# Kernel optimization log

Hardware: AMD Instinct MI355X
Metric: run time of the kernel (lower is better)

Reference implementation:

```python
import jax, jax.numpy as jnp
import numpy as np

N_EMBD = 1024
BLOCK_SIZE = 128
HEAD_SIZE = 128
THETA = 10000.0


def setup_inputs() -> dict:
    key = jax.random.key(0)
    k1, k2, k3, k4 = jax.random.split(key, 4)
    B, T = 256, BLOCK_SIZE
    x = jax.random.normal(k1, (B, T, N_EMBD), dtype=jnp.float32)
    # nn.Linear(n_embd, head_size, bias=False) stored as [n_embd, head_size] so y = x @ W
    s = 1.0 / np.sqrt(N_EMBD)
    Wq = jax.random.normal(k2, (N_EMBD, HEAD_SIZE), dtype=jnp.float32) * s
    Wk = jax.random.normal(k3, (N_EMBD, HEAD_SIZE), dtype=jnp.float32) * s
    Wv = jax.random.normal(k4, (N_EMBD, HEAD_SIZE), dtype=jnp.float32) * s
    return {"x": x, "Wq": Wq, "Wk": Wk, "Wv": Wv}


def _rope_cos_sin(T: int, head_size: int):
    # freqs = exp(arange(0, hs, 2) * (-log(theta)/hs)); angles = outer(t, freqs)
    inv_freq = jnp.exp(jnp.arange(0, head_size, 2, dtype=jnp.float32) * (-np.log(THETA) / head_size))
    angles = jnp.arange(T, dtype=jnp.float32)[:, None] * inv_freq[None, :]  # [T, hs/2]
    return jnp.cos(angles), jnp.sin(angles)


def _apply_rope(t, cos, sin):
    # complex-view rotation on interleaved (even, odd) pairs of the last dim
    tr = t[..., 0::2]  # real parts  [B,T,hs/2]
    ti = t[..., 1::2]  # imag parts
    out_r = tr * cos - ti * sin
    out_i = tr * sin + ti * cos
    return jnp.stack([out_r, out_i], axis=-1).reshape(t.shape)


def reference(x, Wq, Wk, Wv):
    B, T, _ = x.shape
    hs = Wq.shape[1]
    q = x @ Wq  # [B,T,hs]
    k = x @ Wk
    v = x @ Wv
    cos, sin = _rope_cos_sin(T, hs)
    q = _apply_rope(q, cos, sin)
    k = _apply_rope(k, cos, sin)
    scores = jnp.einsum('btd,bsd->bts', q, k) / jnp.sqrt(jnp.asarray(hs, q.dtype))
    causal = jnp.tril(jnp.ones((T, T), dtype=bool))
    scores = jnp.where(causal[None, :, :], scores, -jnp.inf)
    att = jax.nn.softmax(scores, axis=-1)  # dropout is identity in eval
    return jnp.einsum('bts,bsd->btd', att, v)
```

## Files before the change

kernel.cpp:

```cpp
#include <hip/hip_runtime.h>
#include <math.h>

typedef __bf16 bf16x8 __attribute__((ext_vector_type(8)));
typedef float  f32x4  __attribute__((ext_vector_type(4)));
typedef unsigned short us4 __attribute__((ext_vector_type(4)));

constexpr int N_EMBD = 1024;
constexpr int T_SEQ  = 128;
constexpr int HS     = 128;
constexpr int BATCH  = 256;
constexpr int ROWS   = BATCH * T_SEQ;

__device__ __forceinline__ void async16(const void* g, void* l) {
    __builtin_amdgcn_global_load_lds(
        (const __attribute__((address_space(1))) unsigned int*)g,
        (__attribute__((address_space(3))) unsigned int*)l, 16, 0, 0);
}
__device__ __forceinline__ unsigned short bfbits(float f) {
    return __builtin_bit_cast(unsigned short, (__bf16)f);
}
__device__ __forceinline__ f32x4 zero4() {
    f32x4 z = {0.f, 0.f, 0.f, 0.f};
    return z;
}

__global__ __launch_bounds__(256) void wcast(
    const float* __restrict__ Wq, const float* __restrict__ Wk,
    const float* __restrict__ Wv, unsigned short* __restrict__ Wt)
{
    __shared__ unsigned short tile[64][130];
    const int bid = blockIdx.x;
    const int nt  = bid >> 4;
    const int k0  = (bid & 15) << 6;
    const float* src = (nt == 0) ? Wq : ((nt == 1) ? Wk : Wv);
    const int tid = threadIdx.x;
#pragma unroll
    for (int j = 0; j < 32; ++j) {
        int idx = tid + j * 256;
        int k = idx >> 7, n = idx & 127;
        tile[k][n] = bfbits(src[(size_t)(k0 + k) * HS + n]);
    }
    __syncthreads();
#pragma unroll
    for (int j = 0; j < 32; ++j) {
        int idx = tid + j * 256;
        int n = idx >> 6, kk = idx & 63;
        Wt[(size_t)(nt * 128 + n) * N_EMBD + k0 + kk] = tile[kk][n];
    }
}

__global__ __launch_bounds__(512, 2) void head_fused(
    const float* __restrict__ x,
    const unsigned short* __restrict__ Wt,
    float* __restrict__ out)
{
    __shared__ char lds[139264];
    constexpr int QS = 0;
    constexpr int KS = 34816;
    constexpr int VS = 69632;
    constexpr int STG_A = 104448;
    constexpr int STG_B = 114688;

    const int tid  = threadIdx.x;
    const int w    = tid >> 6;
    const int l    = tid & 63;
    const int cl   = l & 15;
    const int quad = l >> 4;
    const int b    = blockIdx.x;
    const int row0 = b << 7;
    const int wm   = (w & 1) << 6;
    const int wn   = (w >> 1) * 96;

    const int arow = tid >> 2;
    const int acol = (tid & 3) << 3;
    const float* aptr = x + (size_t)(row0 + arow) * N_EMBD + acol;
    const int bsrc = (l & 3) ^ quad;

    f32x4 acc[4][6];
#pragma unroll
    for (int a = 0; a < 4; ++a)
#pragma unroll
        for (int c = 0; c < 6; ++c) acc[a][c] = zero4();

    f32x4 a0 = *(const f32x4*)(aptr);
    f32x4 a1 = *(const f32x4*)(aptr + 4);

    for (int kc = 0; kc < N_EMBD; kc += 32) {
        __syncthreads();
        bf16x8 aw;
        aw[0] = (__bf16)a0[0]; aw[1] = (__bf16)a0[1];
        aw[2] = (__bf16)a0[2]; aw[3] = (__bf16)a0[3];
        aw[4] = (__bf16)a1[0]; aw[5] = (__bf16)a1[1];
        aw[6] = (__bf16)a1[2]; aw[7] = (__bf16)a1[3];
        *(bf16x8*)(lds + STG_A + arow * 80 + (tid & 3) * 16) = aw;
#pragma unroll
        for (int jj = 0; jj < 3; ++jj) {
            int j = w * 3 + jj;
            int n = j * 16 + (l >> 2);
            async16(Wt + (size_t)n * N_EMBD + kc + bsrc * 8,
                    lds + STG_B + j * 1024 + 0);
        }
        __syncthreads();
        if (kc + 32 < N_EMBD) {
            a0 = *(const f32x4*)(aptr + kc + 32);
            a1 = *(const f32x4*)(aptr + kc + 36);
        }
        bf16x8 af[4], bf[6];
#pragma unroll
        for (int rt = 0; rt < 4; ++rt) {
            int m = wm + rt * 16 + cl;
            af[rt] = *(const bf16x8*)(lds + STG_A + m * 80 + quad * 16);
        }
#pragma unroll
        for (int ct = 0; ct < 6; ++ct) {
            int n = wn + ct * 16 + cl;
            bf[ct] = *(const bf16x8*)(lds + STG_B + n * 64 + ((quad ^ ((n >> 2) & 3)) << 4));
        }
#pragma unroll
        for (int rt = 0; rt < 4; ++rt)
#pragma unroll
            for (int ct = 0; ct < 6; ++ct)
                acc[rt][ct] = __builtin_amdgcn_mfma_f32_16x16x32_bf16(
                    af[rt], bf[ct], acc[rt][ct], 0, 0, 0);
    }

    const float LNT = 0.07195578430905272f;
#pragma unroll
    for (int ct = 0; ct < 6; ++ct) {
        int c0  = wn + ct * 16;
        int ntc = c0 >> 7;
        int d   = (c0 & 127) + cl;
        if (ntc < 2) {
            int qk = (ntc == 0) ? QS : KS;
            float freq = __expf(-(float)(d & ~1) * LNT);
#pragma unroll
            for (int rt = 0; rt < 4; ++rt) {
#pragma unroll
                for (int i = 0; i < 4; ++i) {
                    int t = wm + rt * 16 + quad * 4 + i;
                    float v = acc[rt][ct][i];
                    float p = __shfl_xor(v, 1);
                    float sn, cs;
                    __sincosf((float)t * freq, &sn, &cs);
                    float r = ((d & 1) == 0) ? (v * cs - p * sn) : (p * sn + v * cs);
                    *(unsigned short*)(lds + qk + t * 272 + d * 2) = bfbits(r);
                }
            }
        } else {
#pragma unroll
            for (int rt = 0; rt < 4; ++rt) {
                int s0 = wm + rt * 16 + quad * 4;
                us4 u;
                u.x = bfbits(acc[rt][ct][0]);
                u.y = bfbits(acc[rt][ct][1]);
                u.z = bfbits(acc[rt][ct][2]);
                u.w = bfbits(acc[rt][ct][3]);
                *(us4*)(lds + VS + d * 272 + s0 * 2) = u;
            }
        }
    }
    __syncthreads();

    const int nct = w + 1;
    const int nks = (w + 2) >> 1;
    char* pl = lds + STG_A + w * 4352;

    bf16x8 qf[4];
#pragma unroll
    for (int ks = 0; ks < 4; ++ks)
        qf[ks] = *(const bf16x8*)(lds + QS + (w * 16 + cl) * 272 + (ks * 4 + quad) * 16);

    f32x4 s[8];
#pragma unroll
    for (int ct = 0; ct < 8; ++ct) s[ct] = zero4();

#pragma unroll
    for (int ct = 0; ct < 8; ++ct) if (ct < nct) {
        const char* kr = lds + KS + (ct * 16 + cl) * 272;
#pragma unroll
        for (int ks = 0; ks < 4; ++ks) {
            bf16x8 bb = *(const bf16x8*)(kr + (ks * 4 + quad) * 16);
            s[ct] = __builtin_amdgcn_mfma_f32_16x16x32_bf16(qf[ks], bb, s[ct], 0, 0, 0);
        }
    }

    const float scale = 0.08838834764831845f;
#pragma unroll
    for (int i = 0; i < 4; ++i) {
        int t = w * 16 + quad * 4 + i;
        float mx = -3.0e38f;
#pragma unroll
        for (int ct = 0; ct < 8; ++ct) if (ct < nct) {
            int col = ct * 16 + cl;
            float v = s[ct][i] * scale;
            v = (col <= t) ? v : -INFINITY;
            s[ct][i] = v;
            mx = fmaxf(mx, v);
        }
        mx = fmaxf(mx, __shfl_xor(mx, 1));
        mx = fmaxf(mx, __shfl_xor(mx, 2));
        mx = fmaxf(mx, __shfl_xor(mx, 4));
        mx = fmaxf(mx, __shfl_xor(mx, 8));
        float sum = 0.f;
#pragma unroll
        for (int ct = 0; ct < 8; ++ct) if (ct < nct) {
            float p = __expf(s[ct][i] - mx);
            s[ct][i] = p;
            sum += p;
        }
        sum += __shfl_xor(sum, 1);
        sum += __shfl_xor(sum, 2);
        sum += __shfl_xor(sum, 4);
        sum += __shfl_xor(sum, 8);
        float inv = 1.0f / sum;
        int rl = quad * 4 + i;
#pragma unroll
        for (int ct = 0; ct < 8; ++ct) if (ct < nct) {
            *(unsigned short*)(pl + rl * 272 + (ct * 16 + cl) * 2) =
                bfbits(s[ct][i] * inv);
        }
        if ((w & 1) == 0) {
            *(unsigned short*)(pl + rl * 272 + (nct * 16 + cl) * 2) = 0;
        }
    }

    bf16x8 ap[4];
#pragma unroll
    for (int ks = 0; ks < 4; ++ks) if (ks < nks)
        ap[ks] = *(const bf16x8*)(pl + cl * 272 + (ks * 4 + quad) * 16);

    f32x4 o[8];
#pragma unroll
    for (int ct = 0; ct < 8; ++ct) o[ct] = zero4();

#pragma unroll
    for (int ct = 0; ct < 8; ++ct) {
        const char* vr = lds + VS + (ct * 16 + cl) * 272;
#pragma unroll
        for (int ks = 0; ks < 4; ++ks) if (ks < nks) {
            bf16x8 bb = *(const bf16x8*)(vr + (ks * 4 + quad) * 16);
            o[ct] = __builtin_amdgcn_mfma_f32_16x16x32_bf16(ap[ks], bb, o[ct], 0, 0, 0);
        }
    }

#pragma unroll
    for (int ct = 0; ct < 8; ++ct)
#pragma unroll
        for (int i = 0; i < 4; ++i) {
            int t = w * 16 + quad * 4 + i;
            out[(size_t)b * 16384 + (size_t)t * HS + ct * 16 + cl] = o[ct][i];
        }
}

extern "C" void kernel_launch(void* const* d_in, const int* in_sizes, int n_in,
                              void* d_out, int out_size, void* d_ws, size_t ws_size,
                              hipStream_t stream) {
    const float* x  = (const float*)d_in[0];
    const float* Wq = (const float*)d_in[1];
    const float* Wk = (const float*)d_in[2];
    const float* Wv = (const float*)d_in[3];
    float* out = (float*)d_out;

    unsigned short* Wt = (unsigned short*)d_ws;

    wcast<<<48, 256, 0, stream>>>(Wq, Wk, Wv, Wt);
    head_fused<<<BATCH, 512, 0, stream>>>(x, Wt, out);
}
```

Measured before the change: 228.4 us.

## Double-buffer the QKV projection GEMM with a 64-wide K step and prefetch

The fused QKV projection loop now uses a 64-element K step with double-buffered LDS tiles for x and the weights. The next weight tile is fetched with async global-to-LDS loads, and the next x tile is loaded into registers while MFMAs run on the current buffers. This leaves one barrier per iteration instead of two and widens the XOR swizzle of the weight tile. The aim is to hide global-load latency, since there is roughly one block per CU. The cost is more LDS (the staging buffers now overlap the Q/K/V regions) and more live registers for the prefetched data.

```diff
diff --git a/kernel.cpp b/kernel.cpp
--- a/kernel.cpp
+++ b/kernel.cpp
@@ -55,11 +55,12 @@
     float* __restrict__ out)
 {
     __shared__ char lds[139264];
-    constexpr int QS = 0;
-    constexpr int KS = 34816;
-    constexpr int VS = 69632;
-    constexpr int STG_A = 104448;
-    constexpr int STG_B = 114688;
+    constexpr int AST = 0,     ASZ = 18432;
+    constexpr int BST = 36864, BSZ = 49152;
+    constexpr int QS  = 0;
+    constexpr int KS  = 34816;
+    constexpr int VS  = 69632;
+    constexpr int PST = 104448;
 
     const int tid  = threadIdx.x;
     const int w    = tid >> 6;
@@ -71,10 +72,11 @@
     const int wm   = (w & 1) << 6;
     const int wn   = (w >> 1) * 96;
 
-    const int arow = tid >> 2;
-    const int acol = (tid & 3) << 3;
-    const float* aptr = x + (size_t)(row0 + arow) * N_EMBD + acol;
-    const int bsrc = (l & 3) ^ quad;
+    const int ar = tid >> 3;
+    const int ac = (tid & 7) << 3;
+    const float* aptr = x + (size_t)row0 * N_EMBD;
+    const int brow = l >> 3;
+    const int bxo  = ((l & 7) ^ brow) << 3;
 
     f32x4 acc[4][6];
 #pragma unroll
@@ -82,46 +84,88 @@
 #pragma unroll
         for (int c = 0; c < 6; ++c) acc[a][c] = zero4();
 
-    f32x4 a0 = *(const f32x4*)(aptr);
-    f32x4 a1 = *(const f32x4*)(aptr + 4);
-
-    for (int kc = 0; kc < N_EMBD; kc += 32) {
+    {
+#pragma unroll
+        for (int jj = 0; jj < 6; ++jj) {
+            int n = w * 48 + jj * 8 + brow;
+            async16(Wt + (size_t)n * N_EMBD + bxo,
+                    lds + BST + (w * 6 + jj) * 1024);
+        }
+        f32x4 p0[2], p1[2];
+#pragma unroll
+        for (int rr = 0; rr < 2; ++rr) {
+            const float* p = aptr + (size_t)(ar + rr * 64) * N_EMBD + ac;
+            p0[rr] = *(const f32x4*)p;
+            p1[rr] = *(const f32x4*)(p + 4);
+        }
+#pragma unroll
+        for (int rr = 0; rr < 2; ++rr) {
+            bf16x8 aw;
+            aw[0] = (__bf16)p0[rr][0]; aw[1] = (__bf16)p0[rr][1];
+            aw[2] = (__bf16)p0[rr][2]; aw[3] = (__bf16)p0[rr][3];
+            aw[4] = (__bf16)p1[rr][0]; aw[5] = (__bf16)p1[rr][1];
+            aw[6] = (__bf16)p1[rr][2]; aw[7] = (__bf16)p1[rr][3];
+            *(bf16x8*)(lds + AST + (ar + rr * 64) * 144 + ac * 2) = aw;
+        }
         __syncthreads();
-        bf16x8 aw;
-        aw[0] = (__bf16)a0[0]; aw[1] = (__bf16)a0[1];
-        aw[2] = (__bf16)a0[2]; aw[3] = (__bf16)a0[3];
-        aw[4] = (__bf16)a1[0]; aw[5] = (__bf16)a1[1];
-        aw[6] = (__bf16)a1[2]; aw[7] = (__bf16)a1[3];
-        *(bf16x8*)(lds + STG_A + arow * 80 + (tid & 3) * 16) = aw;
-#pragma unroll
-        for (int jj = 0; jj < 3; ++jj) {
-            int j = w * 3 + jj;
-            int n = j * 16 + (l >> 2);
-            async16(Wt + (size_t)n * N_EMBD + kc + bsrc * 8,
-                    lds + STG_B + j * 1024 + 0);
+    }
+
+    int cur = 0;
+#pragma unroll 2
+    for (int t = 0; t < 16; ++t) {
+        const int kc = (t + 1) << 6;
+        f32x4 p0[2], p1[2];
+        if (t < 15) {
+#pragma unroll
+            for (int rr = 0; rr < 2; ++rr) {
+                const float* p = aptr + (size_t)(ar + rr * 64) * N_EMBD + kc + ac;
+                p0[rr] = *(const f32x4*)p;
+                p1[rr] = *(const f32x4*)(p + 4);
+            }
+#pragma unroll
+            for (int jj = 0; jj < 6; ++jj) {
+                int n = w * 48 + jj * 8 + brow;
+                async16(Wt + (size_t)n * N_EMBD + kc + bxo,
+                        lds + BST + (cur ^ 1) * BSZ + (w * 6 + jj) * 1024);
+            }
+        }
+        const char* Ab = lds + AST + cur * ASZ;
+        const char* Bb = lds + BST + cur * BSZ;
+#pragma unroll
+        for (int ks2 = 0; ks2 < 2; ++ks2) {
+            bf16x8 af[4], bf[6];
+#pragma unroll
+            for (int rt = 0; rt < 4; ++rt)
+                af[rt] = *(const bf16x8*)(Ab + (wm + rt * 16 + cl) * 144
+                                          + ks2 * 64 + quad * 16);
+#pragma unroll
+            for (int ct = 0; ct < 6; ++ct) {
+                int n = wn + ct * 16 + cl;
+                bf[ct] = *(const bf16x8*)(Bb + n * 128
+                                          + (((ks2 * 4 + quad) ^ (n & 7)) << 4));
+            }
+#pragma unroll
+            for (int rt = 0; rt < 4; ++rt)
+#pragma unroll
+                for (int ct = 0; ct < 6; ++ct)
+                    acc[rt][ct] = __builtin_amdgcn_mfma_f32_16x16x32_bf16(
+                        af[rt], bf[ct], acc[rt][ct], 0, 0, 0);
+        }
+        if (t < 15) {
+            __builtin_amdgcn_sched_barrier(0);
+            char* An = lds + AST + (cur ^ 1) * ASZ;
+#pragma unroll
+            for (int rr = 0; rr < 2; ++rr) {
+                bf16x8 aw;
+                aw[0] = (__bf16)p0[rr][0]; aw[1] = (__bf16)p0[rr][1];
+                aw[2] = (__bf16)p0[rr][2]; aw[3] = (__bf16)p0[rr][3];
+                aw[4] = (__bf16)p1[rr][0]; aw[5] = (__bf16)p1[rr][1];
+                aw[6] = (__bf16)p1[rr][2]; aw[7] = (__bf16)p1[rr][3];
+                *(bf16x8*)(An + (ar + rr * 64) * 144 + ac * 2) = aw;
+            }
         }
         __syncthreads();
-        if (kc + 32 < N_EMBD) {
-            a0 = *(const f32x4*)(aptr + kc + 32);
-            a1 = *(const f32x4*)(aptr + kc + 36);
-        }
-        bf16x8 af[4], bf[6];
-#pragma unroll
-        for (int rt = 0; rt < 4; ++rt) {
-            int m = wm + rt * 16 + cl;
-            af[rt] = *(const bf16x8*)(lds + STG_A + m * 80 + quad * 16);
-        }
-#pragma unroll
-        for (int ct = 0; ct < 6; ++ct) {
-            int n = wn + ct * 16 + cl;
-            bf[ct] = *(const bf16x8*)(lds + STG_B + n * 64 + ((quad ^ ((n >> 2) & 3)) << 4));
-        }
-#pragma unroll
-        for (int rt = 0; rt < 4; ++rt)
-#pragma unroll
-            for (int ct = 0; ct < 6; ++ct)
-                acc[rt][ct] = __builtin_amdgcn_mfma_f32_16x16x32_bf16(
-                    af[rt], bf[ct], acc[rt][ct], 0, 0, 0);
+        cur ^= 1;
     }
 
     const float LNT = 0.07195578430905272f;
@@ -163,7 +207,7 @@
 
     const int nct = w + 1;
     const int nks = (w + 2) >> 1;
-    char* pl = lds + STG_A + w * 4352;
+    char* pl = lds + PST + w * 4352;
 
     bf16x8 qf[4];
 #pragma unroll
```

Measured after the change: 224.1 us. About the same (-1.9%).

## Split fused head kernel into double-buffered QKV+RoPE GEMM and separate attention kernel

Applied to the files above, without the earlier changes.

Splits the single fused per-batch kernel into two kernels. The first computes the QKV projection with RoPE over 64-row halves, using double-buffered LDS staging that prefetches the next K chunk during the MFMAs, and writes Q, K and transposed V to workspace as bf16. The second computes attention over 512 blocks of 4 waves, each wave handling one 16-row query segment and reading Q/K/V straight from global memory. This doubles the grid size and cuts LDS use to raise occupancy and overlap loads, at the cost of an extra kernel launch and a round trip of Q/K/V through global memory.

```diff
diff --git a/kernel.cpp b/kernel.cpp
--- a/kernel.cpp
+++ b/kernel.cpp
@@ -9,7 +9,6 @@
 constexpr int T_SEQ  = 128;
 constexpr int HS     = 128;
 constexpr int BATCH  = 256;
-constexpr int ROWS   = BATCH * T_SEQ;
 
 __device__ __forceinline__ void async16(const void* g, void* l) {
     __builtin_amdgcn_global_load_lds(
@@ -49,32 +48,32 @@
     }
 }
 
-__global__ __launch_bounds__(512, 2) void head_fused(
+__global__ __launch_bounds__(256, 2) void qkv_rope(
     const float* __restrict__ x,
     const unsigned short* __restrict__ Wt,
-    float* __restrict__ out)
+    unsigned short* __restrict__ qr,
+    unsigned short* __restrict__ kr,
+    unsigned short* __restrict__ vT)
 {
-    __shared__ char lds[139264];
-    constexpr int QS = 0;
-    constexpr int KS = 34816;
-    constexpr int VS = 69632;
-    constexpr int STG_A = 104448;
-    constexpr int STG_B = 114688;
+    __shared__ char lds[59392];
+    constexpr int AST = 0,     ASZ = 5120;
+    constexpr int BST = 10240, BSZ = 24576;
 
     const int tid  = threadIdx.x;
     const int w    = tid >> 6;
     const int l    = tid & 63;
     const int cl   = l & 15;
     const int quad = l >> 4;
-    const int b    = blockIdx.x;
-    const int row0 = b << 7;
-    const int wm   = (w & 1) << 6;
-    const int wn   = (w >> 1) * 96;
-
-    const int arow = tid >> 2;
-    const int acol = (tid & 3) << 3;
-    const float* aptr = x + (size_t)(row0 + arow) * N_EMBD + acol;
-    const int bsrc = (l & 3) ^ quad;
+    const int bx   = blockIdx.x;
+    const int b    = bx >> 1;
+    const int half = bx & 1;
+    const int row0 = b * 128 + half * 64;
+
+    const int ar = tid >> 2;
+    const int ac = (tid & 3) << 3;
+    const float* aptr = x + (size_t)(row0 + ar) * N_EMBD + ac;
+    const int brow = l >> 2;
+    const int bxo  = ((l & 3) ^ (brow & 3)) << 3;
 
     f32x4 acc[4][6];
 #pragma unroll
@@ -82,39 +81,49 @@
 #pragma unroll
         for (int c = 0; c < 6; ++c) acc[a][c] = zero4();
 
-    f32x4 a0 = *(const f32x4*)(aptr);
-    f32x4 a1 = *(const f32x4*)(aptr + 4);
-
-    for (int kc = 0; kc < N_EMBD; kc += 32) {
-        __syncthreads();
+    {
+#pragma unroll
+        for (int jj = 0; jj < 6; ++jj) {
+            int n = w * 96 + jj * 16 + brow;
+            async16(Wt + (size_t)n * N_EMBD + bxo,
+                    lds + BST + (w * 96 + jj * 16) * 64);
+        }
+        f32x4 a0 = *(const f32x4*)(aptr);
+        f32x4 a1 = *(const f32x4*)(aptr + 4);
         bf16x8 aw;
         aw[0] = (__bf16)a0[0]; aw[1] = (__bf16)a0[1];
         aw[2] = (__bf16)a0[2]; aw[3] = (__bf16)a0[3];
         aw[4] = (__bf16)a1[0]; aw[5] = (__bf16)a1[1];
         aw[6] = (__bf16)a1[2]; aw[7] = (__bf16)a1[3];
-        *(bf16x8*)(lds + STG_A + arow * 80 + (tid & 3) * 16) = aw;
-#pragma unroll
-        for (int jj = 0; jj < 3; ++jj) {
-            int j = w * 3 + jj;
-            int n = j * 16 + (l >> 2);
-            async16(Wt + (size_t)n * N_EMBD + kc + bsrc * 8,
-                    lds + STG_B + j * 1024 + 0);
-        }
+        *(bf16x8*)(lds + AST + ar * 80 + (tid & 3) * 16) = aw;
         __syncthreads();
-        if (kc + 32 < N_EMBD) {
-            a0 = *(const f32x4*)(aptr + kc + 32);
-            a1 = *(const f32x4*)(aptr + kc + 36);
-        }
+    }
+
+    int cur = 0;
+#pragma unroll 2
+    for (int t = 0; t < 32; ++t) {
+        const int kc = (t + 1) << 5;
+        f32x4 p0, p1;
+        if (t < 31) {
+            p0 = *(const f32x4*)(aptr + kc);
+            p1 = *(const f32x4*)(aptr + kc + 4);
+#pragma unroll
+            for (int jj = 0; jj < 6; ++jj) {
+                int n = w * 96 + jj * 16 + brow;
+                async16(Wt + (size_t)n * N_EMBD + kc + bxo,
+                        lds + BST + (cur ^ 1) * BSZ + (w * 96 + jj * 16) * 64);
+            }
+        }
+        const char* Ab = lds + AST + cur * ASZ;
+        const char* Bb = lds + BST + cur * BSZ;
         bf16x8 af[4], bf[6];
 #pragma unroll
-        for (int rt = 0; rt < 4; ++rt) {
-            int m = wm + rt * 16 + cl;
-            af[rt] = *(const bf16x8*)(lds + STG_A + m * 80 + quad * 16);
-        }
+        for (int rt = 0; rt < 4; ++rt)
+            af[rt] = *(const bf16x8*)(Ab + (rt * 16 + cl) * 80 + quad * 16);
 #pragma unroll
         for (int ct = 0; ct < 6; ++ct) {
-            int n = wn + ct * 16 + cl;
-            bf[ct] = *(const bf16x8*)(lds + STG_B + n * 64 + ((quad ^ ((n >> 2) & 3)) << 4));
+            int n = w * 96 + ct * 16 + cl;
+            bf[ct] = *(const bf16x8*)(Bb + n * 64 + ((quad ^ (n & 3)) << 4));
         }
 #pragma unroll
         for (int rt = 0; rt < 4; ++rt)
@@ -122,53 +131,83 @@
             for (int ct = 0; ct < 6; ++ct)
                 acc[rt][ct] = __builtin_amdgcn_mfma_f32_16x16x32_bf16(
                     af[rt], bf[ct], acc[rt][ct], 0, 0, 0);
+        if (t < 31) {
+            __builtin_amdgcn_sched_barrier(0);
+            bf16x8 aw;
+            aw[0] = (__bf16)p0[0]; aw[1] = (__bf16)p0[1];
+            aw[2] = (__bf16)p0[2]; aw[3] = (__bf16)p0[3];
+            aw[4] = (__bf16)p1[0]; aw[5] = (__bf16)p1[1];
+            aw[6] = (__bf16)p1[2]; aw[7] = (__bf16)p1[3];
+            *(bf16x8*)(lds + AST + (cur ^ 1) * ASZ + ar * 80 + (tid & 3) * 16) = aw;
+        }
+        __syncthreads();
+        cur ^= 1;
     }
 
     const float LNT = 0.07195578430905272f;
 #pragma unroll
     for (int ct = 0; ct < 6; ++ct) {
-        int c0  = wn + ct * 16;
+        int c0  = w * 96 + ct * 16;
         int ntc = c0 >> 7;
         int d   = (c0 & 127) + cl;
         if (ntc < 2) {
-            int qk = (ntc == 0) ? QS : KS;
+            unsigned short* dst = ((ntc == 0) ? qr : kr) + (size_t)b * 16384;
             float freq = __expf(-(float)(d & ~1) * LNT);
 #pragma unroll
             for (int rt = 0; rt < 4; ++rt) {
 #pragma unroll
                 for (int i = 0; i < 4; ++i) {
-                    int t = wm + rt * 16 + quad * 4 + i;
+                    int tt = half * 64 + rt * 16 + quad * 4 + i;
                     float v = acc[rt][ct][i];
                     float p = __shfl_xor(v, 1);
                     float sn, cs;
-                    __sincosf((float)t * freq, &sn, &cs);
+                    __sincosf((float)tt * freq, &sn, &cs);
                     float r = ((d & 1) == 0) ? (v * cs - p * sn) : (p * sn + v * cs);
-                    *(unsigned short*)(lds + qk + t * 272 + d * 2) = bfbits(r);
+                    dst[(size_t)tt * HS + d] = bfbits(r);
                 }
             }
         } else {
 #pragma unroll
             for (int rt = 0; rt < 4; ++rt) {
-                int s0 = wm + rt * 16 + quad * 4;
+                int t0 = half * 64 + rt * 16 + quad * 4;
                 us4 u;
                 u.x = bfbits(acc[rt][ct][0]);
                 u.y = bfbits(acc[rt][ct][1]);
                 u.z = bfbits(acc[rt][ct][2]);
                 u.w = bfbits(acc[rt][ct][3]);
-                *(us4*)(lds + VS + d * 272 + s0 * 2) = u;
+                *(us4*)(vT + (size_t)b * 16384 + (size_t)d * T_SEQ + t0) = u;
             }
         }
     }
-    __syncthreads();
-
-    const int nct = w + 1;
-    const int nks = (w + 2) >> 1;
-    char* pl = lds + STG_A + w * 4352;
+}
+
+__global__ __launch_bounds__(256, 2) void attn(
+    const unsigned short* __restrict__ qr,
+    const unsigned short* __restrict__ kr,
+    const unsigned short* __restrict__ vT,
+    float* __restrict__ out)
+{
+    __shared__ char lds[17408];
+    const int tid  = threadIdx.x;
+    const int w    = tid >> 6;
+    const int l    = tid & 63;
+    const int cl   = l & 15;
+    const int quad = l >> 4;
+    const int bx   = blockIdx.x;
+    const int b    = bx & 255;
+    const int seg  = ((bx >> 8) << 2) + w;
+    const int nct  = seg + 1;
+    const int nks  = (seg + 2) >> 1;
+    char* pl = lds + w * 4352;
+
+    const unsigned short* qb = qr + (size_t)b * 16384;
+    const unsigned short* kb = kr + (size_t)b * 16384;
+    const unsigned short* vb = vT + (size_t)b * 16384;
 
     bf16x8 qf[4];
 #pragma unroll
     for (int ks = 0; ks < 4; ++ks)
-        qf[ks] = *(const bf16x8*)(lds + QS + (w * 16 + cl) * 272 + (ks * 4 + quad) * 16);
+        qf[ks] = *(const bf16x8*)(qb + (seg * 16 + cl) * HS + ks * 32 + quad * 8);
 
     f32x4 s[8];
 #pragma unroll
@@ -176,18 +215,17 @@
 
 #pragma unroll
     for (int ct = 0; ct < 8; ++ct) if (ct < nct) {
-        const char* kr = lds + KS + (ct * 16 + cl) * 272;
 #pragma unroll
         for (int ks = 0; ks < 4; ++ks) {
-            bf16x8 bb = *(const bf16x8*)(kr + (ks * 4 + quad) * 16);
-            s[ct] = __builtin_amdgcn_mfma_f32_16x16x32_bf16(qf[ks], bb, s[ct], 0, 0, 0);
+            bf16x8 kk = *(const bf16x8*)(kb + (ct * 16 + cl) * HS + ks * 32 + quad * 8);
+            s[ct] = __builtin_amdgcn_mfma_f32_16x16x32_bf16(qf[ks], kk, s[ct], 0, 0, 0);
         }
     }
 
     const float scale = 0.08838834764831845f;
 #pragma unroll
     for (int i = 0; i < 4; ++i) {
-        int t = w * 16 + quad * 4 + i;
+        int t = seg * 16 + quad * 4 + i;
         float mx = -3.0e38f;
 #pragma unroll
         for (int ct = 0; ct < 8; ++ct) if (ct < nct) {
@@ -219,7 +257,7 @@
             *(unsigned short*)(pl + rl * 272 + (ct * 16 + cl) * 2) =
                 bfbits(s[ct][i] * inv);
         }
-        if ((w & 1) == 0) {
+        if ((seg & 1) == 0) {
             *(unsigned short*)(pl + rl * 272 + (nct * 16 + cl) * 2) = 0;
         }
     }
@@ -235,11 +273,10 @@
 
 #pragma unroll
     for (int ct = 0; ct < 8; ++ct) {
-        const char* vr = lds + VS + (ct * 16 + cl) * 272;
 #pragma unroll
         for (int ks = 0; ks < 4; ++ks) if (ks < nks) {
-            bf16x8 bb = *(const bf16x8*)(vr + (ks * 4 + quad) * 16);
-            o[ct] = __builtin_amdgcn_mfma_f32_16x16x32_bf16(ap[ks], bb, o[ct], 0, 0, 0);
+            bf16x8 vv = *(const bf16x8*)(vb + (ct * 16 + cl) * T_SEQ + ks * 32 + quad * 8);
+            o[ct] = __builtin_amdgcn_mfma_f32_16x16x32_bf16(ap[ks], vv, o[ct], 0, 0, 0);
         }
     }
 
@@ -247,7 +284,7 @@
     for (int ct = 0; ct < 8; ++ct)
 #pragma unroll
         for (int i = 0; i < 4; ++i) {
-            int t = w * 16 + quad * 4 + i;
+            int t = seg * 16 + quad * 4 + i;
             out[(size_t)b * 16384 + (size_t)t * HS + ct * 16 + cl] = o[ct][i];
         }
 }
@@ -261,8 +298,13 @@
     const float* Wv = (const float*)d_in[3];
     float* out = (float*)d_out;
 
-    unsigned short* Wt = (unsigned short*)d_ws;
+    char* ws = (char*)d_ws;
+    unsigned short* Wt = (unsigned short*)ws;
+    unsigned short* q  = (unsigned short*)(ws + (1  << 20));
+    unsigned short* k  = (unsigned short*)(ws + (9  << 20));
+    unsigned short* vT = (unsigned short*)(ws + (17 << 20));
 
     wcast<<<48, 256, 0, stream>>>(Wq, Wk, Wv, Wt);
-    head_fused<<<BATCH, 512, 0, stream>>>(x, Wt, out);
-}
+    qkv_rope<<<512, 256, 0, stream>>>(x, Wt, q, k, vT);
+    attn<<<512, 256, 0, stream>>>(q, k, vT, out);
+}
```

Result: slower. 248.1 us (+8.6%).
